# Optimization experiments

Hardware: AMD Instinct MI355X
Metric: run time of the kernel (lower is better)

Reference implementation:

```python
import jax, jax.numpy as jnp
import numpy as np

# ---- configuration matching init_kwargs ----
CTX_C = 96        # context_v_features
M_FREQS = 8       # m_encode_num_freqs
OUT_C = 45        # out_features
NDIM = 3
SIGMA = 5.0       # sigma_encode_scale
EPS = 1e-7        # TARGET_COORD_EPSILON
CX = CY = CZ = 32
QX = QY = QZ = 48
B = 1
CTX_VOX = 2.0
Q_VOX = 1.25
N_COORD = 4 * NDIM + NDIM * 2 * M_FREQS   # 60
INTERNAL = CTX_C + N_COORD                # 156


def _lin_init(k, fi, fo):
    s = 1.0 / np.sqrt(fi)
    kw, kb = jax.random.split(k)
    return (jax.random.uniform(kw, (fi, fo), jnp.float32, -s, s),
            jax.random.uniform(kb, (fo,), jnp.float32, -s, s))


def setup_inputs() -> dict:
    key = jax.random.key(0)
    ks = jax.random.split(key, 12)
    context_v = jax.random.normal(ks[0], (B, CTX_C, CX, CY, CZ), jnp.float32)
    ax = jnp.arange(CX, dtype=jnp.float32) * CTX_VOX
    gx, gy, gz = jnp.meshgrid(ax, ax, ax, indexing='ij')
    context_spatial_extent = jnp.broadcast_to(
        jnp.stack([gx, gy, gz], 0)[None], (B, 3, CX, CY, CZ)).astype(jnp.float32)
    # queries in the interior so nearest-idx + 1 stays in bounds
    query_coord = jax.random.uniform(ks[1], (B, 3, QX, QY, QZ), jnp.float32,
                                     CTX_VOX, (CX - 2) * CTX_VOX)
    query_vox_size = jnp.full((B, 3), Q_VOX, jnp.float32)
    inp = dict(context_v=context_v, context_spatial_extent=context_spatial_extent,
               query_vox_size=query_vox_size, query_coord=query_coord)
    ki = 2
    for b in range(2):
        inp[f'blk{b}_w0'], inp[f'blk{b}_b0'] = _lin_init(ks[ki], INTERNAL, CTX_C); ki += 1
        inp[f'blk{b}_w1'], inp[f'blk{b}_b1'] = _lin_init(ks[ki], CTX_C, CTX_C); ki += 1
        inp[f'blk{b}_w2'], inp[f'blk{b}_b2'] = _lin_init(ks[ki], CTX_C, CTX_C); ki += 1
    inp['post_w'], inp['post_b'] = _lin_init(ks[ki], CTX_C, OUT_C)
    return inp


def _flat(t):
    # 'b c x y z -> (b x y z) c'
    return jnp.moveaxis(t, 1, -1).reshape(-1, t.shape[1])


def _unflat(t, b, x, y, z):
    # '(b x y z) c -> b c x y z'
    return jnp.moveaxis(t.reshape(b, x, y, z, -1), -1, 1)


def _fourier(c):
    # c: (N, 3) normalized coords; geometric frequency ladder scaled by sigma
    freqs = SIGMA ** (jnp.arange(M_FREQS, dtype=c.dtype) / M_FREQS)   # (m,)
    ang = (2.0 * jnp.pi) * c[:, :, None] * freqs                      # (N,3,m)
    return jnp.concatenate([jnp.sin(ang), jnp.cos(ang)], axis=-1).reshape(c.shape[0], -1)


def _skip_block(x, coord, w0, b0, w1, b1, w2, b2):
    # SkipMLPBlock: concat(context, coord) -> 3 dense SiLU layers -> residual add
    h = jnp.concatenate([x, coord], axis=-1)
    h = jax.nn.silu(h @ w0 + b0)
    h = jax.nn.silu(h @ w1 + b1)
    h = jax.nn.silu(h @ w2 + b2)
    return x + h, coord


def _sub_grid_forward(ctx_val, ctx_coord, q_coord, ctx_vox, q_vox, p):
    # ctx_val: (B,C,X,Y,Z); coords: (B,3,X,Y,Z); ctx_vox/q_vox: (B,3,1,1,1)
    b, _, x, y, z = q_coord.shape
    rel = jnp.maximum(ctx_coord - q_coord, -ctx_vox / 2 + EPS)
    rel_norm = (rel - jnp.min(rel, axis=(2, 3, 4), keepdims=True)) / (1.5 * ctx_vox)
    enc = _fourier(_flat(rel_norm))                                   # (N, 6m)
    qv = jnp.broadcast_to(q_vox, rel_norm.shape)
    coord_feats = jnp.concatenate(
        [_flat(qv), _flat(ctx_coord), _flat(q_coord), _flat(rel_norm), enc], axis=-1)
    h = _flat(ctx_val)
    xc = coord_feats
    for i in range(2):
        h, xc = _skip_block(h, xc, p[f'blk{i}_w0'], p[f'blk{i}_b0'],
                            p[f'blk{i}_w1'], p[f'blk{i}_b1'],
                            p[f'blk{i}_w2'], p[f'blk{i}_b2'])
    pred = h @ p['post_w'] + p['post_b']
    return _unflat(pred, b, x, y, z), rel


def reference(context_v, context_spatial_extent, query_vox_size, query_coord,
              blk0_w0, blk0_b0, blk0_w1, blk0_b1, blk0_w2, blk0_b2,
              blk1_w0, blk1_b0, blk1_w1, blk1_b1, blk1_w2, blk1_b2,
              post_w, post_b):
    p = dict(blk0_w0=blk0_w0, blk0_b0=blk0_b0, blk0_w1=blk0_w1, blk0_b1=blk0_b1,
             blk0_w2=blk0_w2, blk0_b2=blk0_b2, blk1_w0=blk1_w0, blk1_b0=blk1_b0,
             blk1_w1=blk1_w1, blk1_b1=blk1_b1, blk1_w2=blk1_w2, blk1_b2=blk1_b2,
             post_w=post_w, post_b=post_b)
    bsz, _, qx, qy, qz = query_coord.shape
    cx, cy, cz = context_spatial_extent.shape[2:]
    ctx_vox = jnp.abs(context_spatial_extent[..., 1, 1, 1]
                      - context_spatial_extent[..., 0, 0, 0])[:, :, None, None, None]
    q_vox = query_vox_size[:, :, None, None, None]
    # nearest context voxel index per query point (regular grid)
    origin = context_spatial_extent[:, :, 0, 0, 0][:, :, None, None, None]
    nearest = jnp.round((query_coord - origin) / ctx_vox).astype(jnp.int32)
    xi = jnp.clip(nearest[:, 0], 0, cx - 2).reshape(-1)
    yi = jnp.clip(nearest[:, 1], 0, cy - 2).reshape(-1)
    zi = jnp.clip(nearest[:, 2], 0, cz - 2).reshape(-1)
    b_idx = jnp.broadcast_to(jnp.arange(bsz)[:, None, None, None],
                             (bsz, qx, qy, qz)).reshape(-1)
    preds = []
    rel000 = None
    for i in (0, 1):
        for j in (0, 1):
            for k in (0, 1):
                cval = context_v[b_idx, :, xi + i, yi + j, zi + k]            # (N,C) gather
                cval = _unflat(cval, bsz, qx, qy, qz)
                ccoord = context_spatial_extent[b_idx, :, xi + i, yi + j, zi + k]
                ccoord = _unflat(ccoord, bsz, qx, qy, qz)
                pred, rel = _sub_grid_forward(cval, ccoord, query_coord,
                                              ctx_vox, q_vox, p)
                preds.append(pred)
                if i == 0 and j == 0 and k == 0:
                    rel000 = rel
    preds = jnp.stack(preds, 0)   # (8, B, OUT, X, Y, Z)
    # trilinear combine over the 2x2x2 sub-window (grid_sample align_corners=True;
    # grid coord channel 0 indexes z_sub (W), 1 -> y_sub (H), 2 -> x_sub (D))
    g = jnp.clip((rel000 - 0.5) * 2.0, -1.0 + EPS, 1.0 - EPS)
    t = (g + 1.0) / 2.0
    tz, ty, tx = t[:, 0], t[:, 1], t[:, 2]
    out = jnp.zeros_like(preds[0])
    for i in (0, 1):
        wi = tx if i == 1 else 1.0 - tx
        for j in (0, 1):
            wj = ty if j == 1 else 1.0 - ty
            for k in (0, 1):
                wk = tz if k == 1 else 1.0 - tz
                out = out + preds[i * 4 + j * 2 + k] * (wi * wj * wk)[:, None]
    return out
```

## Files before the change

kernel.cpp:

```cpp
#include <hip/hip_runtime.h>
#include <hip/hip_bf16.h>

typedef unsigned short ushort_t;
typedef short short8 __attribute__((ext_vector_type(8)));
typedef float floatx4 __attribute__((ext_vector_type(4)));

#define SA 168
#define SW 104
#define NQ 110592
#define CVOL 32768

#define L0A 0
#define L1A 15360
#define L2A 24576
#define L0B 33792
#define L1B 49152
#define L2B 58368
#define PST 67584
#define WTOT 72192

#if __has_builtin(__builtin_amdgcn_sinf) && __has_builtin(__builtin_amdgcn_cosf) && __has_builtin(__builtin_amdgcn_fractf)
#define FAST_SINCOS 1
#else
#define FAST_SINCOS 0
#endif

__device__ __forceinline__ float bf2f(ushort_t u) { return __uint_as_float(((unsigned)u) << 16); }
__device__ __forceinline__ ushort_t f2bf(float f) {
    unsigned u = __float_as_uint(f);
    unsigned r = (u + 0x7fffu + ((u >> 16) & 1u)) >> 16;
    return (ushort_t)r;
}
__device__ __forceinline__ unsigned encodeMin(float x) {
    unsigned u = __float_as_uint(x);
    return (u & 0x80000000u) ? ~u : (u | 0x80000000u);
}
__device__ __forceinline__ float decodeMin(unsigned key) {
    unsigned u = (key & 0x80000000u) ? (key ^ 0x80000000u) : ~key;
    return __uint_as_float(u);
}

__device__ __constant__ float FREQ[8] = {
    1.0f, 1.2228445f, 1.4953488f, 1.8285791f,
    2.2360680f, 2.7343640f, 3.3437015f, 4.0888269f
};

__global__ void decoder_txp(const float* __restrict__ cv, ushort_t* __restrict__ cvT) {
    __shared__ ushort_t ld[128 * SW];
    int tid = threadIdx.x;
    int base = blockIdx.x * 128;
    int cl = tid & 127, h = tid >> 7;
    #pragma unroll 4
    for (int ch = h * 48; ch < h * 48 + 48; ++ch)
        ld[cl * SW + ch] = f2bf(cv[ch * CVOL + base + cl]);
    __syncthreads();
    #pragma unroll
    for (int it = 0; it < 6; ++it) {
        int idx = it * 256 + tid;
        int r = idx / 12, c = idx - r * 12;
        *(uint4*)&cvT[(base + r) * 96 + c * 8] = *(const uint4*)&ld[r * SW + c * 8];
    }
}

__global__ void decoder_prep(const float* __restrict__ w00, const float* __restrict__ w01,
                             const float* __restrict__ w02, const float* __restrict__ w10,
                             const float* __restrict__ w11, const float* __restrict__ w12,
                             const float* __restrict__ pw, ushort_t* __restrict__ wsW,
                             unsigned* __restrict__ keys) {
    int idx = blockIdx.x * 256 + threadIdx.x;
    if (idx < 3) keys[idx] = 0xFFFFFFFFu;
    if (idx >= WTOT) return;
    const float* W; int K, N, fo, nkc, off;
    if (idx < L1A)      { W = w00; K = 156; N = 96; fo = 96; nkc = 5; off = L0A; }
    else if (idx < L2A) { W = w01; K = 96;  N = 96; fo = 96; nkc = 3; off = L1A; }
    else if (idx < L0B) { W = w02; K = 96;  N = 96; fo = 96; nkc = 3; off = L2A; }
    else if (idx < L1B) { W = w10; K = 156; N = 96; fo = 96; nkc = 5; off = L0B; }
    else if (idx < L2B) { W = w11; K = 96;  N = 96; fo = 96; nkc = 3; off = L1B; }
    else if (idx < PST) { W = w12; K = 96;  N = 96; fo = 96; nkc = 3; off = L2B; }
    else                { W = pw;  K = 96;  N = 45; fo = 45; nkc = 3; off = PST; }
    int li = idx - off;
    int j = li & 7, lane = (li >> 3) & 63, chunk = li >> 9;
    int kc = chunk % nkc, t = chunk / nkc;
    int k = kc * 32 + (lane >> 4) * 8 + j;
    int n = t * 16 + (lane & 15);
    wsW[idx] = (k < K && n < N) ? f2bf(W[k * fo + n]) : (ushort_t)0;
}

__global__ void decoder_prepass(const float* __restrict__ qc, const float* __restrict__ ext,
                                unsigned* __restrict__ keys) {
    __shared__ unsigned mk[3];
    int tid = threadIdx.x;
    int lane = tid & 63;
    if (tid < 3) mk[tid] = 0xFFFFFFFFu;
    __syncthreads();
    int p = blockIdx.x * 256 + tid;
    #pragma unroll
    for (int c = 0; c < 3; ++c) {
        float org = ext[c * CVOL];
        float vox = fabsf(ext[c * CVOL + 1057] - org);
        float q = qc[c * NQ + p];
        float nf = rintf((q - org) / vox);
        int ci = (int)nf; ci = ci < 0 ? 0 : (ci > 30 ? 30 : ci);
        float base = org + (float)ci * vox - q;
        for (int off = 32; off > 0; off >>= 1) base = fminf(base, __shfl_xor(base, off));
        if (lane == 0) atomicMin(&mk[c], encodeMin(base));
    }
    __syncthreads();
    if (tid < 3) atomicMin(&keys[tid], mk[tid]);
}

template <int NKC>
__device__ __forceinline__ void layer_gemm(const ushort_t* __restrict__ wb,
                                           const ushort_t* XinP, int wn3, int lane8, int quad8,
                                           floatx4 acc[4][3]) {
    short8 bfr[NKC][3];
    #pragma unroll
    for (int nt = 0; nt < 3; ++nt)
        #pragma unroll
        for (int kc = 0; kc < NKC; ++kc)
            bfr[kc][nt] = *(const short8*)&wb[(((wn3 + nt) * NKC + kc) << 9) + lane8];
    #pragma unroll
    for (int mt = 0; mt < 4; ++mt)
        #pragma unroll
        for (int nt = 0; nt < 3; ++nt) acc[mt][nt] = (floatx4){0.f, 0.f, 0.f, 0.f};
    #pragma unroll
    for (int kc = 0; kc < NKC; ++kc) {
        short8 a[4];
        #pragma unroll
        for (int mt = 0; mt < 4; ++mt)
            a[mt] = *(const short8*)&XinP[mt * 16 * SA + kc * 32 + quad8];
        #pragma unroll
        for (int nt = 0; nt < 3; ++nt)
            #pragma unroll
            for (int mt = 0; mt < 4; ++mt)
                acc[mt][nt] = __builtin_amdgcn_mfma_f32_16x16x32_bf16(a[mt], bfr[kc][nt], acc[mt][nt], 0, 0, 0);
    }
}

__global__ __launch_bounds__(256, 3) void decoder_main(
    const ushort_t* __restrict__ cvT, const float* __restrict__ ext,
    const float* __restrict__ qvx, const float* __restrict__ qc,
    const float* __restrict__ b00, const float* __restrict__ b01, const float* __restrict__ b02,
    const float* __restrict__ b10, const float* __restrict__ b11, const float* __restrict__ b12,
    const float* __restrict__ pb, const ushort_t* __restrict__ wsW,
    const unsigned* __restrict__ minKeys, float* __restrict__ out)
{
    __shared__ ushort_t Xin[128 * SA];
    __shared__ ushort_t Hhat[16 * SW];
    __shared__ float ptQ[3][16], ptBase[3][16], ptT[3][16];
    __shared__ int ptCI[3][16];
    __shared__ float wcorn[16][8];

    const int tid = threadIdx.x;
    const int lane = tid & 63;
    const int wv = tid >> 6;
    const int quad = lane >> 4;
    const int l16 = lane & 15;
    const int wm = wv & 1, wn = wv >> 1;
    const int wn3 = wn * 3, lane8 = lane << 3, quad8 = quad * 8;
    const int p0 = blockIdx.x * 16;

    float vox[3], org[3], lim[3], inv3v[3], qv[3], mrel[3][2];
    #pragma unroll
    for (int c = 0; c < 3; ++c) {
        org[c] = ext[c * CVOL];
        vox[c] = fabsf(ext[c * CVOL + 1057] - org[c]);
        lim[c] = -0.5f * vox[c] + 1e-7f;
        inv3v[c] = 1.0f / (1.5f * vox[c]);
        qv[c] = qvx[c];
        float mb = decodeMin(minKeys[c]);
        mrel[c][0] = fmaxf(mb, lim[c]);
        mrel[c][1] = fmaxf(mb + vox[c], lim[c]);
    }

    if (tid < 64) {
        int p = tid >> 2, c = tid & 3;
        if (c < 3) {
            float q = qc[c * NQ + p0 + p];
            float nf = rintf((q - org[c]) / vox[c]);
            int ci = (int)nf; ci = ci < 0 ? 0 : (ci > 30 ? 30 : ci);
            float base = org[c] + (float)ci * vox[c] - q;
            float rel0 = fmaxf(base, lim[c]);
            float g = fminf(fmaxf((rel0 - 0.5f) * 2.0f, -1.0f + 1e-7f), 1.0f - 1e-7f);
            ptQ[c][p] = q; ptCI[c][p] = ci; ptBase[c][p] = base; ptT[c][p] = (g + 1.0f) * 0.5f;
        }
    }
    __syncthreads();

    if (tid < 128) {
        int p = tid >> 3, corner = tid & 7;
        int i = corner >> 2, j = (corner >> 1) & 1, k = corner & 1;
        float wx = i ? ptT[2][p] : 1.0f - ptT[2][p];
        float wy = j ? ptT[1][p] : 1.0f - ptT[1][p];
        float wz = k ? ptT[0][p] : 1.0f - ptT[0][p];
        wcorn[p][corner] = wx * wy * wz;
    }

    {
        const int r = tid >> 1, h = tid & 1;
        const int p = r >> 3, corner = r & 7;
        const int i0 = corner >> 2, i1 = (corner >> 1) & 1, i2 = corner & 1;
        int io[3] = {i0, i1, i2};

        int cell = (ptCI[0][p] + i0) * 1024 + (ptCI[1][p] + i1) * 32 + ptCI[2][p] + i2;
        const uint4* src = (const uint4*)&cvT[cell * 96];
        uint4* dstX = (uint4*)&Xin[r * SA];
        #pragma unroll
        for (int cc = h * 6; cc < h * 6 + 6; ++cc) dstX[cc] = src[cc];

        float rn[3];
        #pragma unroll
        for (int c = 0; c < 3; ++c) {
            float rel = fmaxf(ptBase[c][p] + (float)io[c] * vox[c], lim[c]);
            rn[c] = (rel - mrel[c][io[c]]) * inv3v[c];
        }
        ushort_t* row = &Xin[r * SA];
        if (h == 0) {
            #pragma unroll
            for (int c = 0; c < 3; ++c) {
                row[96 + c]  = f2bf(qv[c]);
                row[99 + c]  = f2bf(org[c] + (float)(ptCI[c][p] + io[c]) * vox[c]);
                row[102 + c] = f2bf(ptQ[c][p]);
                row[105 + c] = f2bf(rn[c]);
            }
            #pragma unroll
            for (int z = 156; z < SA; ++z) row[z] = 0;
            #pragma unroll
            for (int m = 0; m < 8; ++m) {
                float ang = rn[0] * FREQ[m];
#if FAST_SINCOS
                float fr = __builtin_amdgcn_fractf(ang);
                row[108 + m] = f2bf(__builtin_amdgcn_sinf(fr));
                row[116 + m] = f2bf(__builtin_amdgcn_cosf(fr));
#else
                float s, co; sincospif(2.0f * ang, &s, &co);
                row[108 + m] = f2bf(s); row[116 + m] = f2bf(co);
#endif
            }
        } else {
            #pragma unroll
            for (int c = 1; c < 3; ++c) {
                #pragma unroll
                for (int m = 0; m < 8; ++m) {
                    float ang = rn[c] * FREQ[m];
#if FAST_SINCOS
                    float fr = __builtin_amdgcn_fractf(ang);
                    row[108 + c * 16 + m] = f2bf(__builtin_amdgcn_sinf(fr));
                    row[108 + c * 16 + 8 + m] = f2bf(__builtin_amdgcn_cosf(fr));
#else
                    float s, co; sincospif(2.0f * ang, &s, &co);
                    row[108 + c * 16 + m] = f2bf(s);
                    row[108 + c * 16 + 8 + m] = f2bf(co);
#endif
                }
            }
        }
    }
    __syncthreads();

    const ushort_t* XinP = &Xin[(64 * wm + l16) * SA];
    const int wboff[2][3] = {{L0A, L1A, L2A}, {L0B, L1B, L2B}};
    const float* const bptr[2][3] = {{b00, b01, b02}, {b10, b11, b12}};
    float hold[4][3][4];
    floatx4 acc[4][3];

    #pragma unroll
    for (int blk = 0; blk < 2; ++blk) {
        if (blk == 0) {
            #pragma unroll
            for (int mt = 0; mt < 4; ++mt)
                #pragma unroll
                for (int nt = 0; nt < 3; ++nt)
                    #pragma unroll
                    for (int r = 0; r < 4; ++r)
                        hold[mt][nt][r] = bf2f(Xin[(64 * wm + 16 * mt + quad * 4 + r) * SA + 48 * wn + 16 * nt + l16]);
        }

        #pragma unroll
        for (int l = 0; l < 3; ++l) {
            if (l == 0) layer_gemm<5>(wsW + wboff[blk][0], XinP, wn3, lane8, quad8, acc);
            else        layer_gemm<3>(wsW + wboff[blk][l], XinP, wn3, lane8, quad8, acc);

            const float* bias = bptr[blk][l];
            ushort_t hb[4][3][4];
            #pragma unroll
            for (int nt = 0; nt < 3; ++nt) {
                float bv = bias[48 * wn + 16 * nt + l16];
                #pragma unroll
                for (int mt = 0; mt < 4; ++mt)
                    #pragma unroll
                    for (int r = 0; r < 4; ++r) {
                        float z = acc[mt][nt][r] + bv;
                        float s = z * __builtin_amdgcn_rcpf(1.0f + __expf(-z));
                        if (l == 2) {
                            s += hold[mt][nt][r];
                            ushort_t u = f2bf(s);
                            hb[mt][nt][r] = u;
                            hold[mt][nt][r] = bf2f(u);
                        } else {
                            hb[mt][nt][r] = f2bf(s);
                        }
                    }
            }
            __syncthreads();
            #pragma unroll
            for (int mt = 0; mt < 4; ++mt)
                #pragma unroll
                for (int nt = 0; nt < 3; ++nt)
                    #pragma unroll
                    for (int r = 0; r < 4; ++r)
                        Xin[(64 * wm + 16 * mt + quad * 4 + r) * SA + 48 * wn + 16 * nt + l16] = hb[mt][nt][r];
            __syncthreads();
        }
    }

    {
        int p = tid >> 4, s6 = (tid & 15) * 6;
        float w8[8];
        #pragma unroll
        for (int c = 0; c < 8; ++c) w8[c] = wcorn[p][c];
        #pragma unroll
        for (int cc = 0; cc < 6; ++cc) {
            int col = s6 + cc;
            float sum = 0.f;
            #pragma unroll
            for (int c = 0; c < 8; ++c) sum += w8[c] * bf2f(Xin[(p * 8 + c) * SA + col]);
            Hhat[p * SW + col] = f2bf(sum);
        }
    }
    __syncthreads();

    if (wv < 3) {
        const ushort_t* wb = wsW + PST;
        floatx4 pacc = (floatx4){0.f, 0.f, 0.f, 0.f};
        #pragma unroll
        for (int kc = 0; kc < 3; ++kc) {
            short8 a = *(const short8*)&Hhat[l16 * SW + kc * 32 + quad8];
            short8 bfrag = *(const short8*)&wb[(((wv * 3) + kc) << 9) + lane8];
            pacc = __builtin_amdgcn_mfma_f32_16x16x32_bf16(a, bfrag, pacc, 0, 0, 0);
        }
        int n = 16 * wv + l16;
        if (n < 45) {
            float bv = pb[n];
            float4 v;
            v.x = pacc[0] + bv; v.y = pacc[1] + bv; v.z = pacc[2] + bv; v.w = pacc[3] + bv;
            *(float4*)&out[n * NQ + p0 + quad * 4] = v;
        }
    }
}

extern "C" void kernel_launch(void* const* d_in, const int* in_sizes, int n_in,
                              void* d_out, int out_size, void* d_ws, size_t ws_size,
                              hipStream_t stream) {
    (void)in_sizes; (void)n_in; (void)out_size; (void)ws_size;
    const float* cv  = (const float*)d_in[0];
    const float* ext = (const float*)d_in[1];
    const float* qvx = (const float*)d_in[2];
    const float* qc  = (const float*)d_in[3];
    const float* w00 = (const float*)d_in[4];
    const float* b00 = (const float*)d_in[5];
    const float* w01 = (const float*)d_in[6];
    const float* b01 = (const float*)d_in[7];
    const float* w02 = (const float*)d_in[8];
    const float* b02 = (const float*)d_in[9];
    const float* w10 = (const float*)d_in[10];
    const float* b10 = (const float*)d_in[11];
    const float* w11 = (const float*)d_in[12];
    const float* b11 = (const float*)d_in[13];
    const float* w12 = (const float*)d_in[14];
    const float* b12 = (const float*)d_in[15];
    const float* pw  = (const float*)d_in[16];
    const float* pb  = (const float*)d_in[17];

    unsigned* keys = (unsigned*)d_ws;
    ushort_t* wsW  = (ushort_t*)((char*)d_ws + 64);
    ushort_t* cvT  = (ushort_t*)((char*)d_ws + 163840);

    decoder_txp<<<256, 256, 0, stream>>>(cv, cvT);
    decoder_prep<<<282, 256, 0, stream>>>(w00, w01, w02, w10, w11, w12, pw, wsW, keys);
    decoder_prepass<<<432, 256, 0, stream>>>(qc, ext, keys);
    decoder_main<<<6912, 256, 0, stream>>>(cvT, ext, qvx, qc,
                                           b00, b01, b02, b10, b11, b12,
                                           pb, wsW, keys, (float*)d_out);
}
```

Baseline: 377.4 us.

## Keep MLP activations in registers by transposing GEMMs and chaining MFMA outputs

The per-layer MLP GEMMs are transposed so weights become the A operand and activations the B operand, with each wave owning 32 point columns. Outputs of layer 0 and layer 1 are packed straight into 16x16x16 MFMA B fragments in registers, with no round trip through shared memory and no block-wide barriers between layers. Only the residual layer reads and writes Xin, and it touches just the wave's own columns. Biases are pre-laid-out in fragment order by the prep kernel. The cost is more registers (6x2 accumulators plus fragments) and weights re-read from global or L2 per wave, which could lower occupancy under the 3-block launch bound.

```diff
diff --git a/kernel.cpp b/kernel.cpp
--- a/kernel.cpp
+++ b/kernel.cpp
@@ -3,6 +3,9 @@
 
 typedef unsigned short ushort_t;
 typedef short short8 __attribute__((ext_vector_type(8)));
+typedef short shrt4 __attribute__((ext_vector_type(4)));
+typedef unsigned short ush4 __attribute__((ext_vector_type(4)));
+typedef unsigned int uintx2 __attribute__((ext_vector_type(2)));
 typedef float floatx4 __attribute__((ext_vector_type(4)));
 
 #define SA 168
@@ -10,16 +13,27 @@
 #define NQ 110592
 #define CVOL 32768
 
-#define L0A 0
-#define L1A 15360
-#define L2A 24576
-#define L0B 33792
-#define L1B 49152
-#define L2B 58368
-#define PST 67584
-#define WTOT 72192
-
-#if __has_builtin(__builtin_amdgcn_sinf) && __has_builtin(__builtin_amdgcn_cosf) && __has_builtin(__builtin_amdgcn_fractf)
+#define L0A   0
+#define L0B   15360
+#define A1_00 30720
+#define A1_01 39936
+#define A1_10 49152
+#define A1_11 58368
+#define PST   67584
+#define WTOT  72192
+#define BTOT  9216
+
+#define WSW_OFF  64
+#define BIAS_OFF 147456
+#define CVT_OFF  196608
+
+#if defined(__HIP_DEVICE_COMPILE__)
+#define MFMA16(A, B, C) __builtin_amdgcn_mfma_f32_16x16x16bf16_1k(A, B, C, 0, 0, 0)
+#else
+#define MFMA16(A, B, C) (C)
+#endif
+
+#if defined(__HIP_DEVICE_COMPILE__) && __has_builtin(__builtin_amdgcn_sinf) && __has_builtin(__builtin_amdgcn_cosf) && __has_builtin(__builtin_amdgcn_fractf)
 #define FAST_SINCOS 1
 #else
 #define FAST_SINCOS 0
@@ -30,6 +44,12 @@
     unsigned u = __float_as_uint(f);
     unsigned r = (u + 0x7fffu + ((u >> 16) & 1u)) >> 16;
     return (ushort_t)r;
+}
+__device__ __forceinline__ shrt4 pk4(floatx4 v) {
+    uintx2 u;
+    u[0] = (unsigned)f2bf(v[0]) | ((unsigned)f2bf(v[1]) << 16);
+    u[1] = (unsigned)f2bf(v[2]) | ((unsigned)f2bf(v[3]) << 16);
+    return __builtin_bit_cast(shrt4, u);
 }
 __device__ __forceinline__ unsigned encodeMin(float x) {
     unsigned u = __float_as_uint(x);
@@ -62,28 +82,55 @@
     }
 }
 
-__global__ void decoder_prep(const float* __restrict__ w00, const float* __restrict__ w01,
-                             const float* __restrict__ w02, const float* __restrict__ w10,
-                             const float* __restrict__ w11, const float* __restrict__ w12,
+__global__ void decoder_prep(const float* __restrict__ w00, const float* __restrict__ b00,
+                             const float* __restrict__ w01, const float* __restrict__ b01,
+                             const float* __restrict__ w02, const float* __restrict__ b02,
+                             const float* __restrict__ w10, const float* __restrict__ b10,
+                             const float* __restrict__ w11, const float* __restrict__ b11,
+                             const float* __restrict__ w12, const float* __restrict__ b12,
                              const float* __restrict__ pw, ushort_t* __restrict__ wsW,
-                             unsigned* __restrict__ keys) {
+                             float* __restrict__ biasF, unsigned* __restrict__ keys) {
     int idx = blockIdx.x * 256 + threadIdx.x;
     if (idx < 3) keys[idx] = 0xFFFFFFFFu;
-    if (idx >= WTOT) return;
-    const float* W; int K, N, fo, nkc, off;
-    if (idx < L1A)      { W = w00; K = 156; N = 96; fo = 96; nkc = 5; off = L0A; }
-    else if (idx < L2A) { W = w01; K = 96;  N = 96; fo = 96; nkc = 3; off = L1A; }
-    else if (idx < L0B) { W = w02; K = 96;  N = 96; fo = 96; nkc = 3; off = L2A; }
-    else if (idx < L1B) { W = w10; K = 156; N = 96; fo = 96; nkc = 5; off = L0B; }
-    else if (idx < L2B) { W = w11; K = 96;  N = 96; fo = 96; nkc = 3; off = L1B; }
-    else if (idx < PST) { W = w12; K = 96;  N = 96; fo = 96; nkc = 3; off = L2B; }
-    else                { W = pw;  K = 96;  N = 45; fo = 45; nkc = 3; off = PST; }
-    int li = idx - off;
-    int j = li & 7, lane = (li >> 3) & 63, chunk = li >> 9;
-    int kc = chunk % nkc, t = chunk / nkc;
-    int k = kc * 32 + (lane >> 4) * 8 + j;
-    int n = t * 16 + (lane & 15);
-    wsW[idx] = (k < K && n < N) ? f2bf(W[k * fo + n]) : (ushort_t)0;
+    if (idx >= WTOT + BTOT) return;
+    if (idx >= WTOT) {
+        int t = idx - WTOT;
+        int layer = t / 1536, rem = t - layer * 1536;
+        int mt = rem >> 8, l2i = rem & 255;
+        int lane = l2i >> 2, r = l2i & 3;
+        int m = mt * 16 + (lane >> 4) * 4 + r;
+        const float* B = layer == 0 ? b00 : layer == 1 ? b01 : layer == 2 ? b02
+                       : layer == 3 ? b10 : layer == 4 ? b11 : b12;
+        biasF[t] = B[m];
+        return;
+    }
+    ushort_t v = 0;
+    if (idx < A1_00) {
+        const float* W = (idx < L0B) ? w00 : w10;
+        int li = idx - ((idx < L0B) ? L0A : L0B);
+        int j = li & 7, lane = (li >> 3) & 63, chunk = li >> 9;
+        int kc = chunk % 5, mt = chunk / 5;
+        int k = kc * 32 + (lane >> 4) * 8 + j;
+        int m = mt * 16 + (lane & 15);
+        if (k < 156) v = f2bf(W[k * 96 + m]);
+    } else if (idx < PST) {
+        const float* W = idx < A1_01 ? w01 : idx < A1_10 ? w02 : idx < A1_11 ? w11 : w12;
+        int off = idx < A1_01 ? A1_00 : idx < A1_10 ? A1_01 : idx < A1_11 ? A1_10 : A1_11;
+        int li = idx - off;
+        int i = li & 3, kl = (li >> 2) & 1, lane = (li >> 3) & 63, chunk = li >> 9;
+        int kp = chunk % 3, mt = chunk / 3;
+        int k = (kp * 2 + kl) * 16 + (lane >> 4) * 4 + i;
+        int m = mt * 16 + (lane & 15);
+        v = f2bf(W[k * 96 + m]);
+    } else {
+        int li = idx - PST;
+        int j = li & 7, lane = (li >> 3) & 63, chunk = li >> 9;
+        int kc = chunk % 3, t = chunk / 3;
+        int k = kc * 32 + (lane >> 4) * 8 + j;
+        int n = t * 16 + (lane & 15);
+        if (n < 45) v = f2bf(pw[k * 45 + n]);
+    }
+    wsW[idx] = v;
 }
 
 __global__ void decoder_prepass(const float* __restrict__ qc, const float* __restrict__ ext,
@@ -109,40 +156,11 @@
     if (tid < 3) atomicMin(&keys[tid], mk[tid]);
 }
 
-template <int NKC>
-__device__ __forceinline__ void layer_gemm(const ushort_t* __restrict__ wb,
-                                           const ushort_t* XinP, int wn3, int lane8, int quad8,
-                                           floatx4 acc[4][3]) {
-    short8 bfr[NKC][3];
-    #pragma unroll
-    for (int nt = 0; nt < 3; ++nt)
-        #pragma unroll
-        for (int kc = 0; kc < NKC; ++kc)
-            bfr[kc][nt] = *(const short8*)&wb[(((wn3 + nt) * NKC + kc) << 9) + lane8];
-    #pragma unroll
-    for (int mt = 0; mt < 4; ++mt)
-        #pragma unroll
-        for (int nt = 0; nt < 3; ++nt) acc[mt][nt] = (floatx4){0.f, 0.f, 0.f, 0.f};
-    #pragma unroll
-    for (int kc = 0; kc < NKC; ++kc) {
-        short8 a[4];
-        #pragma unroll
-        for (int mt = 0; mt < 4; ++mt)
-            a[mt] = *(const short8*)&XinP[mt * 16 * SA + kc * 32 + quad8];
-        #pragma unroll
-        for (int nt = 0; nt < 3; ++nt)
-            #pragma unroll
-            for (int mt = 0; mt < 4; ++mt)
-                acc[mt][nt] = __builtin_amdgcn_mfma_f32_16x16x32_bf16(a[mt], bfr[kc][nt], acc[mt][nt], 0, 0, 0);
-    }
-}
-
 __global__ __launch_bounds__(256, 3) void decoder_main(
     const ushort_t* __restrict__ cvT, const float* __restrict__ ext,
     const float* __restrict__ qvx, const float* __restrict__ qc,
-    const float* __restrict__ b00, const float* __restrict__ b01, const float* __restrict__ b02,
-    const float* __restrict__ b10, const float* __restrict__ b11, const float* __restrict__ b12,
     const float* __restrict__ pb, const ushort_t* __restrict__ wsW,
+    const float* __restrict__ biasF,
     const unsigned* __restrict__ minKeys, float* __restrict__ out)
 {
     __shared__ ushort_t Xin[128 * SA];
@@ -156,9 +174,9 @@
     const int wv = tid >> 6;
     const int quad = lane >> 4;
     const int l16 = lane & 15;
-    const int wm = wv & 1, wn = wv >> 1;
-    const int wn3 = wn * 3, lane8 = lane << 3, quad8 = quad * 8;
+    const int lane8 = lane << 3, quad8 = quad * 8, quad4 = quad * 4;
     const int p0 = blockIdx.x * 16;
+    const int col0 = wv * 32;
 
     float vox[3], org[3], lim[3], inv3v[3], qv[3], mrel[3][2];
     #pragma unroll
@@ -258,59 +276,111 @@
     }
     __syncthreads();
 
-    const ushort_t* XinP = &Xin[(64 * wm + l16) * SA];
-    const int wboff[2][3] = {{L0A, L1A, L2A}, {L0B, L1B, L2B}};
-    const float* const bptr[2][3] = {{b00, b01, b02}, {b10, b11, b12}};
-    float hold[4][3][4];
-    floatx4 acc[4][3];
+    const int A32off[2] = {L0A, L0B};
+    const int A16off[2][2] = {{A1_00, A1_01}, {A1_10, A1_11}};
+    floatx4 acc[6][2];
+    shrt4 bfr[6][2];
 
     #pragma unroll
     for (int blk = 0; blk < 2; ++blk) {
-        if (blk == 0) {
-            #pragma unroll
-            for (int mt = 0; mt < 4; ++mt)
-                #pragma unroll
-                for (int nt = 0; nt < 3; ++nt)
+        {
+            short8 bX[2][5];
+            #pragma unroll
+            for (int nt = 0; nt < 2; ++nt)
+                #pragma unroll
+                for (int kc = 0; kc < 5; ++kc)
+                    bX[nt][kc] = *(const short8*)&Xin[(col0 + nt * 16 + l16) * SA + kc * 32 + quad8];
+            #pragma unroll
+            for (int mt = 0; mt < 6; ++mt) {
+                short8 aw[5];
+                #pragma unroll
+                for (int kc = 0; kc < 5; ++kc)
+                    aw[kc] = *(const short8*)&wsW[A32off[blk] + ((mt * 5 + kc) << 9) + lane8];
+                #pragma unroll
+                for (int nt = 0; nt < 2; ++nt) {
+                    floatx4 a = {0.f, 0.f, 0.f, 0.f};
                     #pragma unroll
-                    for (int r = 0; r < 4; ++r)
-                        hold[mt][nt][r] = bf2f(Xin[(64 * wm + 16 * mt + quad * 4 + r) * SA + 48 * wn + 16 * nt + l16]);
-        }
-
-        #pragma unroll
-        for (int l = 0; l < 3; ++l) {
-            if (l == 0) layer_gemm<5>(wsW + wboff[blk][0], XinP, wn3, lane8, quad8, acc);
-            else        layer_gemm<3>(wsW + wboff[blk][l], XinP, wn3, lane8, quad8, acc);
-
-            const float* bias = bptr[blk][l];
-            ushort_t hb[4][3][4];
-            #pragma unroll
-            for (int nt = 0; nt < 3; ++nt) {
-                float bv = bias[48 * wn + 16 * nt + l16];
-                #pragma unroll
-                for (int mt = 0; mt < 4; ++mt)
+                    for (int kc = 0; kc < 5; ++kc)
+                        a = __builtin_amdgcn_mfma_f32_16x16x32_bf16(aw[kc], bX[nt][kc], a, 0, 0, 0);
+                    acc[mt][nt] = a;
+                }
+            }
+        }
+        {
+            const int lay = blk * 3;
+            #pragma unroll
+            for (int mt = 0; mt < 6; ++mt) {
+                floatx4 bv = *(const floatx4*)&biasF[((lay * 6 + mt) << 8) + (lane << 2)];
+                #pragma unroll
+                for (int nt = 0; nt < 2; ++nt) {
+                    floatx4 s;
                     #pragma unroll
                     for (int r = 0; r < 4; ++r) {
-                        float z = acc[mt][nt][r] + bv;
-                        float s = z * __builtin_amdgcn_rcpf(1.0f + __expf(-z));
-                        if (l == 2) {
-                            s += hold[mt][nt][r];
-                            ushort_t u = f2bf(s);
-                            hb[mt][nt][r] = u;
-                            hold[mt][nt][r] = bf2f(u);
-                        } else {
-                            hb[mt][nt][r] = f2bf(s);
+                        float z = acc[mt][nt][r] + bv[r];
+                        s[r] = z * __builtin_amdgcn_rcpf(1.0f + __expf(-z));
+                    }
+                    bfr[mt][nt] = pk4(s);
+                }
+            }
+        }
+        #pragma unroll
+        for (int l = 1; l < 3; ++l) {
+            #pragma unroll
+            for (int mt = 0; mt < 6; ++mt) {
+                short8 awp[3];
+                #pragma unroll
+                for (int kp = 0; kp < 3; ++kp)
+                    awp[kp] = *(const short8*)&wsW[A16off[blk][l - 1] + ((mt * 3 + kp) << 9) + lane8];
+                #pragma unroll
+                for (int nt = 0; nt < 2; ++nt) {
+                    floatx4 a = {0.f, 0.f, 0.f, 0.f};
+                    #pragma unroll
+                    for (int kc = 0; kc < 6; ++kc) {
+                        shrt4 af = (kc & 1)
+                            ? __builtin_shufflevector(awp[kc >> 1], awp[kc >> 1], 4, 5, 6, 7)
+                            : __builtin_shufflevector(awp[kc >> 1], awp[kc >> 1], 0, 1, 2, 3);
+                        a = MFMA16(af, bfr[kc][nt], a);
+                    }
+                    acc[mt][nt] = a;
+                }
+            }
+            const int lay = blk * 3 + l;
+            if (l == 1) {
+                #pragma unroll
+                for (int mt = 0; mt < 6; ++mt) {
+                    floatx4 bv = *(const floatx4*)&biasF[((lay * 6 + mt) << 8) + (lane << 2)];
+                    #pragma unroll
+                    for (int nt = 0; nt < 2; ++nt) {
+                        floatx4 s;
+                        #pragma unroll
+                        for (int r = 0; r < 4; ++r) {
+                            float z = acc[mt][nt][r] + bv[r];
+                            s[r] = z * __builtin_amdgcn_rcpf(1.0f + __expf(-z));
                         }
+                        bfr[mt][nt] = pk4(s);
                     }
-            }
-            __syncthreads();
-            #pragma unroll
-            for (int mt = 0; mt < 4; ++mt)
-                #pragma unroll
-                for (int nt = 0; nt < 3; ++nt)
+                }
+            } else {
+                #pragma unroll
+                for (int mt = 0; mt < 6; ++mt) {
+                    floatx4 bv = *(const floatx4*)&biasF[((lay * 6 + mt) << 8) + (lane << 2)];
                     #pragma unroll
-                    for (int r = 0; r < 4; ++r)
-                        Xin[(64 * wm + 16 * mt + quad * 4 + r) * SA + 48 * wn + 16 * nt + l16] = hb[mt][nt][r];
-            __syncthreads();
+                    for (int nt = 0; nt < 2; ++nt) {
+                        int ca = (col0 + nt * 16 + l16) * SA + mt * 16 + quad4;
+                        ush4 hu = *(const ush4*)&Xin[ca];
+                        floatx4 s;
+                        #pragma unroll
+                        for (int r = 0; r < 4; ++r) {
+                            float z = acc[mt][nt][r] + bv[r];
+                            s[r] = z * __builtin_amdgcn_rcpf(1.0f + __expf(-z)) + bf2f(hu[r]);
+                        }
+                        uintx2 w;
+                        w[0] = (unsigned)f2bf(s[0]) | ((unsigned)f2bf(s[1]) << 16);
+                        w[1] = (unsigned)f2bf(s[2]) | ((unsigned)f2bf(s[3]) << 16);
+                        *(uintx2*)&Xin[ca] = w;
+                    }
+                }
+            }
         }
     }
 
@@ -332,11 +402,11 @@
 
     if (wv < 3) {
         const ushort_t* wb = wsW + PST;
-        floatx4 pacc = (floatx4){0.f, 0.f, 0.f, 0.f};
+        floatx4 pacc = {0.f, 0.f, 0.f, 0.f};
         #pragma unroll
         for (int kc = 0; kc < 3; ++kc) {
             short8 a = *(const short8*)&Hhat[l16 * SW + kc * 32 + quad8];
-            short8 bfrag = *(const short8*)&wb[(((wv * 3) + kc) << 9) + lane8];
+            short8 bfrag = *(const short8*)&wb[((wv * 3 + kc) << 9) + lane8];
             pacc = __builtin_amdgcn_mfma_f32_16x16x32_bf16(a, bfrag, pacc, 0, 0, 0);
         }
         int n = 16 * wv + l16;
@@ -373,13 +443,15 @@
     const float* pb  = (const float*)d_in[17];
 
     unsigned* keys = (unsigned*)d_ws;
-    ushort_t* wsW  = (ushort_t*)((char*)d_ws + 64);
-    ushort_t* cvT  = (ushort_t*)((char*)d_ws + 163840);
+    ushort_t* wsW  = (ushort_t*)((char*)d_ws + WSW_OFF);
+    float* biasF   = (float*)((char*)d_ws + BIAS_OFF);
+    ushort_t* cvT  = (ushort_t*)((char*)d_ws + CVT_OFF);
 
     decoder_txp<<<256, 256, 0, stream>>>(cv, cvT);
-    decoder_prep<<<282, 256, 0, stream>>>(w00, w01, w02, w10, w11, w12, pw, wsW, keys);
+    decoder_prep<<<318, 256, 0, stream>>>(w00, b00, w01, b01, w02, b02,
+                                          w10, b10, w11, b11, w12, b12,
+                                          pw, wsW, biasF, keys);
     decoder_prepass<<<432, 256, 0, stream>>>(qc, ext, keys);
     decoder_main<<<6912, 256, 0, stream>>>(cvT, ext, qvx, qc,
-                                           b00, b01, b02, b10, b11, b12,
-                                           pb, wsW, keys, (float*)d_out);
-}
+                                           pb, wsW, biasF, keys, (float*)d_out);
+}
```

After: 356.7 us. -5.5%, faster.
